# Optimization experiments

Measured on AMD Instinct MI355X. Metric: run time of the kernel, lower is better.

## Reference

```python
import jax, jax.numpy as jnp
import numpy as np

EPS = 1e-8

def setup_inputs() -> dict:
    key = jax.random.key(0)
    k1, k2 = jax.random.split(key)
    B, D, H, W, K = 32, 256, 64, 64, 64
    X = jax.random.normal(k1, (B, D, H, W), dtype=jnp.float32)
    std1 = 1.0 / float(np.sqrt(K * D))
    codewords = jax.random.uniform(k2, (K, D), dtype=jnp.float32, minval=-std1, maxval=std1)
    return {"X": X, "codewords": codewords}

def reference(X, codewords):
    B, D = X.shape[0], X.shape[1]
    # (B, D, H, W) -> (B, N, D)
    Xf = X.reshape(B, D, -1).transpose(0, 2, 1)
    # pairwise cosine similarity: normalize then matmul -> (B, N, K)
    Xn = Xf / jnp.maximum(jnp.linalg.norm(Xf, axis=-1, keepdims=True), EPS)
    Cn = codewords / jnp.maximum(jnp.linalg.norm(codewords, axis=-1, keepdims=True), EPS)
    L = jnp.einsum('bnd,kd->bnk', Xn, Cn)
    A = jax.nn.softmax(L, axis=2)
    # aggregate: E[b,k,d] = sum_n A[b,n,k] * (Xf[b,n,d] - C[k,d])
    # expressed without materializing the (B,N,K,D) residual tensor:
    E = jnp.einsum('bnk,bnd->bkd', A, Xf) - A.sum(axis=1)[:, :, None] * codewords[None, :, :]
    return E
```

## Files before the change

kernel.cpp:

```cpp
#include <hip/hip_runtime.h>
#include <hip/hip_bf16.h>
#include <math.h>

#define BB 32
#define DD 256
#define NN 4096
#define KK 64
#define EPSV 1e-8f
#define XSTR 264

typedef __attribute__((ext_vector_type(8))) short short8;
typedef __attribute__((ext_vector_type(4))) float f32x4;

__device__ __forceinline__ unsigned int bf16pair(float a, float b) {
    __hip_bfloat162 h = __float22bfloat162_rn(make_float2(a, b));
    return *(unsigned int*)&h;
}
__device__ __forceinline__ unsigned short bf16one(float a) {
    unsigned int ua = __float_as_uint(a);
    ua += 0x7fffu + ((ua >> 16) & 1u);
    return (unsigned short)(ua >> 16);
}

__device__ __forceinline__ void stage_group(int dbase, int n4, const float4* rr,
                                            unsigned short* xnd_s, unsigned short* xdn_s,
                                            f32x4& ssn) {
    float4 r0 = rr[0], r1 = rr[1], r2 = rr[2], r3 = rr[3];
    ssn.x = fmaf(r0.x, r0.x, ssn.x); ssn.x = fmaf(r1.x, r1.x, ssn.x);
    ssn.x = fmaf(r2.x, r2.x, ssn.x); ssn.x = fmaf(r3.x, r3.x, ssn.x);
    ssn.y = fmaf(r0.y, r0.y, ssn.y); ssn.y = fmaf(r1.y, r1.y, ssn.y);
    ssn.y = fmaf(r2.y, r2.y, ssn.y); ssn.y = fmaf(r3.y, r3.y, ssn.y);
    ssn.z = fmaf(r0.z, r0.z, ssn.z); ssn.z = fmaf(r1.z, r1.z, ssn.z);
    ssn.z = fmaf(r2.z, r2.z, ssn.z); ssn.z = fmaf(r3.z, r3.z, ssn.z);
    ssn.w = fmaf(r0.w, r0.w, ssn.w); ssn.w = fmaf(r1.w, r1.w, ssn.w);
    ssn.w = fmaf(r2.w, r2.w, ssn.w); ssn.w = fmaf(r3.w, r3.w, ssn.w);
#pragma unroll
    for (int j = 0; j < 4; j++) {
        int d = dbase + j;
        uint2 u;
        u.x = bf16pair(rr[j].x, rr[j].y);
        u.y = bf16pair(rr[j].z, rr[j].w);
        *(uint2*)(xdn_s + d * 64 + ((((n4 >> 3) ^ (d & 7)) << 3) | (n4 & 7))) = u;
    }
    {
        float col[4][4] = {{r0.x, r1.x, r2.x, r3.x},
                           {r0.y, r1.y, r2.y, r3.y},
                           {r0.z, r1.z, r2.z, r3.z},
                           {r0.w, r1.w, r2.w, r3.w}};
#pragma unroll
        for (int j = 0; j < 4; j++) {
            int n = n4 + j;
            uint2 u;
            u.x = bf16pair(col[j][0], col[j][1]);
            u.y = bf16pair(col[j][2], col[j][3]);
            int blk = (dbase >> 3) ^ ((n >> 2) & 3);
            *(uint2*)(xnd_s + n * XSTR + (blk << 3) + (dbase & 7)) = u;
        }
    }
}

__global__ __launch_bounds__(256, 2) void k_fused(const float* __restrict__ X,
                                                  const float* __restrict__ C,
                                                  float* __restrict__ P,
                                                  float* __restrict__ Sp) {
    __shared__ unsigned short xnd_s[64 * XSTR];
    __shared__ unsigned short xdn_s[DD * 64];
    __shared__ unsigned short at_s[KK * 72];
    __shared__ float rn4[4 * 64];
    __shared__ float red_s[4 * 64];

    int t = threadIdx.x;
    int b = blockIdx.x >> 4, chunk = blockIdx.x & 15;
    int w = t >> 6, lane = t & 63, c = lane & 15, g = lane >> 4;
    int q = t >> 4;
    int n4 = c * 4;

    const float* Xb = X + (size_t)b * DD * NN + chunk * 256;

    float4 pre[8];
#pragma unroll
    for (int i = 0; i < 2; i++) {
        const float* xb = Xb + (size_t)(q * 4 + 64 * i) * NN + n4;
#pragma unroll
        for (int j = 0; j < 4; j++) pre[i * 4 + j] = *(const float4*)(xb + (size_t)j * NN);
    }

    short8 cnf[8];
    {
        int k = 16 * w + c;
        const float* cp = C + k * DD;
        float4 v0[8], v1[8];
        float ss = 0.f;
#pragma unroll
        for (int ks = 0; ks < 8; ks++) {
            v0[ks] = *(const float4*)(cp + 32 * ks + 8 * g);
            v1[ks] = *(const float4*)(cp + 32 * ks + 8 * g + 4);
            ss = fmaf(v0[ks].x, v0[ks].x, ss); ss = fmaf(v0[ks].y, v0[ks].y, ss);
            ss = fmaf(v0[ks].z, v0[ks].z, ss); ss = fmaf(v0[ks].w, v0[ks].w, ss);
            ss = fmaf(v1[ks].x, v1[ks].x, ss); ss = fmaf(v1[ks].y, v1[ks].y, ss);
            ss = fmaf(v1[ks].z, v1[ks].z, ss); ss = fmaf(v1[ks].w, v1[ks].w, ss);
        }
        ss += __shfl_xor(ss, 16);
        ss += __shfl_xor(ss, 32);
        float r = 1.f / fmaxf(sqrtf(ss), EPSV);
#pragma unroll
        for (int ks = 0; ks < 8; ks++) {
            uint4 u;
            u.x = bf16pair(v0[ks].x * r, v0[ks].y * r);
            u.y = bf16pair(v0[ks].z * r, v0[ks].w * r);
            u.z = bf16pair(v1[ks].x * r, v1[ks].y * r);
            u.w = bf16pair(v1[ks].z * r, v1[ks].w * r);
            cnf[ks] = *(short8*)&u;
        }
    }

    f32x4 eacc[4][4];
#pragma unroll
    for (int dt = 0; dt < 4; dt++)
#pragma unroll
        for (int kt = 0; kt < 4; kt++) eacc[dt][kt] = (f32x4){0.f, 0.f, 0.f, 0.f};
    float s_acc[4] = {0.f, 0.f, 0.f, 0.f};

    for (int p = 0; p < 4; p++) {
        float4 cur[8];
#pragma unroll
        for (int i = 0; i < 2; i++) {
            const float* xb = Xb + (size_t)(q * 4 + 64 * (2 + i)) * NN + p * 64 + n4;
#pragma unroll
            for (int j = 0; j < 4; j++) cur[i * 4 + j] = *(const float4*)(xb + (size_t)j * NN);
        }
        __syncthreads();

        f32x4 ssn = (f32x4){0.f, 0.f, 0.f, 0.f};
#pragma unroll
        for (int i = 0; i < 2; i++)
            stage_group(q * 4 + 64 * i, n4, &pre[i * 4], xnd_s, xdn_s, ssn);

        if (p < 3) {
#pragma unroll
            for (int i = 0; i < 2; i++) {
                const float* xb = Xb + (size_t)(q * 4 + 64 * i) * NN + (p + 1) * 64 + n4;
#pragma unroll
                for (int j = 0; j < 4; j++) pre[i * 4 + j] = *(const float4*)(xb + (size_t)j * NN);
            }
        }

#pragma unroll
        for (int i = 0; i < 2; i++)
            stage_group(q * 4 + 64 * (2 + i), n4, &cur[i * 4], xnd_s, xdn_s, ssn);

        ssn.x += __shfl_xor(ssn.x, 16); ssn.x += __shfl_xor(ssn.x, 32);
        ssn.y += __shfl_xor(ssn.y, 16); ssn.y += __shfl_xor(ssn.y, 32);
        ssn.z += __shfl_xor(ssn.z, 16); ssn.z += __shfl_xor(ssn.z, 32);
        ssn.w += __shfl_xor(ssn.w, 16); ssn.w += __shfl_xor(ssn.w, 32);
        if (g == 0) *(f32x4*)(rn4 + w * 64 + n4) = ssn;

        __syncthreads();

        f32x4 lacc[4];
#pragma unroll
        for (int nt = 0; nt < 4; nt++) lacc[nt] = (f32x4){0.f, 0.f, 0.f, 0.f};
#pragma unroll
        for (int ks = 0; ks < 8; ks++) {
            short8 af = cnf[ks];
#pragma unroll
            for (int nt = 0; nt < 4; nt++) {
                int n = nt * 16 + c;
                short8 bf = *(const short8*)(xnd_s + n * XSTR +
                                             (((4 * ks + g) ^ ((n >> 2) & 3)) << 3));
                lacc[nt] = __builtin_amdgcn_mfma_f32_16x16x32_bf16(af, bf, lacc[nt], 0, 0, 0);
            }
        }

        float lv[4][4];
#pragma unroll
        for (int nt = 0; nt < 4; nt++) {
            int n = nt * 16 + c;
            float ssq = rn4[n] + rn4[64 + n] + rn4[128 + n] + rn4[192 + n];
            float rn = 1.f / fmaxf(sqrtf(ssq), EPSV);
            float s = 0.f;
#pragma unroll
            for (int r = 0; r < 4; r++) {
                lv[nt][r] = __expf(lacc[nt][r] * rn);
                s += lv[nt][r];
            }
            s += __shfl_xor(s, 16);
            s += __shfl_xor(s, 32);
            if (g == 0) red_s[w * 64 + n] = s;
        }
        __syncthreads();

#pragma unroll
        for (int nt = 0; nt < 4; nt++) {
            int n = nt * 16 + c;
            float denom = red_s[n] + red_s[64 + n] + red_s[128 + n] + red_s[192 + n];
            float inv = 1.f / denom;
#pragma unroll
            for (int r = 0; r < 4; r++) {
                float a = lv[nt][r] * inv;
                s_acc[r] += a;
                int k = 16 * w + 4 * g + r;
                at_s[k * 72 + ((((n >> 3) ^ (k & 7)) << 3) | (n & 7))] = bf16one(a);
            }
        }
        __syncthreads();

#pragma unroll
        for (int ks2 = 0; ks2 < 2; ks2++) {
            short8 bk[4];
#pragma unroll
            for (int kt = 0; kt < 4; kt++) {
                int k = kt * 16 + c;
                bk[kt] = *(const short8*)(at_s + k * 72 + (((4 * ks2 + g) ^ (k & 7)) << 3));
            }
#pragma unroll
            for (int dt = 0; dt < 4; dt++) {
                int d = w * 64 + dt * 16 + c;
                short8 af = *(const short8*)(xdn_s + d * 64 + (((4 * ks2 + g) ^ (d & 7)) << 3));
#pragma unroll
                for (int kt = 0; kt < 4; kt++)
                    eacc[dt][kt] =
                        __builtin_amdgcn_mfma_f32_16x16x32_bf16(af, bk[kt], eacc[dt][kt], 0, 0, 0);
            }
        }
    }

    float* Pb = P + (size_t)blockIdx.x * (DD * KK);
#pragma unroll
    for (int dt = 0; dt < 4; dt++)
#pragma unroll
        for (int kt = 0; kt < 4; kt++) {
            int k = kt * 16 + c;
            int d0 = w * 64 + dt * 16 + 4 * g;
            *(f32x4*)(Pb + (size_t)k * DD + d0) = eacc[dt][kt];
        }
#pragma unroll
    for (int r = 0; r < 4; r++) {
        float v = s_acc[r];
        v += __shfl_xor(v, 1);
        v += __shfl_xor(v, 2);
        v += __shfl_xor(v, 4);
        v += __shfl_xor(v, 8);
        if (c == 0) Sp[blockIdx.x * 64 + 16 * w + 4 * g + r] = v;
    }
}

__global__ __launch_bounds__(256) void k_fin(const float* __restrict__ P,
                                             const float* __restrict__ Sp,
                                             const float* __restrict__ C,
                                             float* __restrict__ out) {
    int idx = blockIdx.x * 256 + threadIdx.x;
    int b = idx >> 12;
    int r = idx & 4095;
    int k = r >> 6;
    int d0 = (r & 63) * 4;
    const float* Pp = P + (size_t)b * 16 * (DD * KK) + k * DD + d0;
    const float* Sb = Sp + b * 16 * 64 + k;
    f32x4 e0 = (f32x4){0.f, 0.f, 0.f, 0.f};
    f32x4 e1 = (f32x4){0.f, 0.f, 0.f, 0.f};
    float s0 = 0.f, s1 = 0.f;
#pragma unroll
    for (int cc = 0; cc < 16; cc += 2) {
        f32x4 p0 = *(const f32x4*)(Pp + (size_t)cc * (DD * KK));
        f32x4 p1 = *(const f32x4*)(Pp + (size_t)(cc + 1) * (DD * KK));
        e0 += p0;
        e1 += p1;
        s0 += Sb[cc * 64];
        s1 += Sb[(cc + 1) * 64];
    }
    f32x4 cv = *(const f32x4*)(C + k * DD + d0);
    f32x4 e = e0 + e1;
    float s = s0 + s1;
    f32x4 o;
    o.x = e.x - s * cv.x;
    o.y = e.y - s * cv.y;
    o.z = e.z - s * cv.z;
    o.w = e.w - s * cv.w;
    *(f32x4*)(out + (size_t)(b * 64 + k) * DD + d0) = o;
}

extern "C" void kernel_launch(void* const* d_in, const int* in_sizes, int n_in,
                              void* d_out, int out_size, void* d_ws, size_t ws_size,
                              hipStream_t stream) {
    const float* X = (const float*)d_in[0];
    const float* C = (const float*)d_in[1];
    float* out = (float*)d_out;
    unsigned char* ws = (unsigned char*)d_ws;

    float* Sp = (float*)ws;
    float* P = (float*)(ws + 131072);

    k_fused<<<512, 256, 0, stream>>>(X, C, P, Sp);
    k_fin<<<512, 256, 0, stream>>>(P, Sp, C, out);
}
```

Baseline: 212.0 us.

## Double threads per block to 512, splitting work across eight waves

```diff
diff --git a/kernel.cpp b/kernel.cpp
--- a/kernel.cpp
+++ b/kernel.cpp
@@ -59,35 +59,35 @@
     }
 }
 
-__global__ __launch_bounds__(256, 2) void k_fused(const float* __restrict__ X,
+__global__ __launch_bounds__(512, 4) void k_fused(const float* __restrict__ X,
                                                   const float* __restrict__ C,
                                                   float* __restrict__ P,
                                                   float* __restrict__ Sp) {
     __shared__ unsigned short xnd_s[64 * XSTR];
     __shared__ unsigned short xdn_s[DD * 64];
     __shared__ unsigned short at_s[KK * 72];
-    __shared__ float rn4[4 * 64];
-    __shared__ float red_s[4 * 64];
+    __shared__ float rn4[8 * 64];
+    __shared__ float red_s[8 * 64];
 
     int t = threadIdx.x;
     int b = blockIdx.x >> 4, chunk = blockIdx.x & 15;
     int w = t >> 6, lane = t & 63, c = lane & 15, g = lane >> 4;
-    int q = t >> 4;
+    int q2 = t >> 4;
     int n4 = c * 4;
+    int kw = w & 3, nh = w >> 2;
 
     const float* Xb = X + (size_t)b * DD * NN + chunk * 256;
 
-    float4 pre[8];
-#pragma unroll
-    for (int i = 0; i < 2; i++) {
-        const float* xb = Xb + (size_t)(q * 4 + 64 * i) * NN + n4;
-#pragma unroll
-        for (int j = 0; j < 4; j++) pre[i * 4 + j] = *(const float4*)(xb + (size_t)j * NN);
+    float4 pre[4];
+    {
+        const float* xb = Xb + (size_t)(q2 * 4) * NN + n4;
+#pragma unroll
+        for (int j = 0; j < 4; j++) pre[j] = *(const float4*)(xb + (size_t)j * NN);
     }
 
     short8 cnf[8];
     {
-        int k = 16 * w + c;
+        int k = 16 * kw + c;
         const float* cp = C + k * DD;
         float4 v0[8], v1[8];
         float ss = 0.f;
@@ -114,40 +114,32 @@
         }
     }
 
-    f32x4 eacc[4][4];
-#pragma unroll
-    for (int dt = 0; dt < 4; dt++)
+    f32x4 eacc[2][4];
+#pragma unroll
+    for (int dt = 0; dt < 2; dt++)
 #pragma unroll
         for (int kt = 0; kt < 4; kt++) eacc[dt][kt] = (f32x4){0.f, 0.f, 0.f, 0.f};
     float s_acc[4] = {0.f, 0.f, 0.f, 0.f};
 
     for (int p = 0; p < 4; p++) {
-        float4 cur[8];
-#pragma unroll
-        for (int i = 0; i < 2; i++) {
-            const float* xb = Xb + (size_t)(q * 4 + 64 * (2 + i)) * NN + p * 64 + n4;
-#pragma unroll
-            for (int j = 0; j < 4; j++) cur[i * 4 + j] = *(const float4*)(xb + (size_t)j * NN);
+        float4 cur[4];
+        {
+            const float* xb = Xb + (size_t)(q2 * 4 + 128) * NN + p * 64 + n4;
+#pragma unroll
+            for (int j = 0; j < 4; j++) cur[j] = *(const float4*)(xb + (size_t)j * NN);
         }
         __syncthreads();
 
         f32x4 ssn = (f32x4){0.f, 0.f, 0.f, 0.f};
-#pragma unroll
-        for (int i = 0; i < 2; i++)
-            stage_group(q * 4 + 64 * i, n4, &pre[i * 4], xnd_s, xdn_s, ssn);
+        stage_group(q2 * 4, n4, pre, xnd_s, xdn_s, ssn);
 
         if (p < 3) {
-#pragma unroll
-            for (int i = 0; i < 2; i++) {
-                const float* xb = Xb + (size_t)(q * 4 + 64 * i) * NN + (p + 1) * 64 + n4;
-#pragma unroll
-                for (int j = 0; j < 4; j++) pre[i * 4 + j] = *(const float4*)(xb + (size_t)j * NN);
-            }
-        }
-
-#pragma unroll
-        for (int i = 0; i < 2; i++)
-            stage_group(q * 4 + 64 * (2 + i), n4, &cur[i * 4], xnd_s, xdn_s, ssn);
+            const float* xb = Xb + (size_t)(q2 * 4) * NN + (p + 1) * 64 + n4;
+#pragma unroll
+            for (int j = 0; j < 4; j++) pre[j] = *(const float4*)(xb + (size_t)j * NN);
+        }
+
+        stage_group(q2 * 4 + 128, n4, cur, xnd_s, xdn_s, ssn);
 
         ssn.x += __shfl_xor(ssn.x, 16); ssn.x += __shfl_xor(ssn.x, 32);
         ssn.y += __shfl_xor(ssn.y, 16); ssn.y += __shfl_xor(ssn.y, 32);
@@ -157,26 +149,27 @@
 
         __syncthreads();
 
-        f32x4 lacc[4];
-#pragma unroll
-        for (int nt = 0; nt < 4; nt++) lacc[nt] = (f32x4){0.f, 0.f, 0.f, 0.f};
+        f32x4 lacc[2];
+#pragma unroll
+        for (int nt = 0; nt < 2; nt++) lacc[nt] = (f32x4){0.f, 0.f, 0.f, 0.f};
 #pragma unroll
         for (int ks = 0; ks < 8; ks++) {
             short8 af = cnf[ks];
 #pragma unroll
-            for (int nt = 0; nt < 4; nt++) {
-                int n = nt * 16 + c;
+            for (int nt = 0; nt < 2; nt++) {
+                int n = 32 * nh + nt * 16 + c;
                 short8 bf = *(const short8*)(xnd_s + n * XSTR +
                                              (((4 * ks + g) ^ ((n >> 2) & 3)) << 3));
                 lacc[nt] = __builtin_amdgcn_mfma_f32_16x16x32_bf16(af, bf, lacc[nt], 0, 0, 0);
             }
         }
 
-        float lv[4][4];
-#pragma unroll
-        for (int nt = 0; nt < 4; nt++) {
-            int n = nt * 16 + c;
-            float ssq = rn4[n] + rn4[64 + n] + rn4[128 + n] + rn4[192 + n];
+        float lv[2][4];
+#pragma unroll
+        for (int nt = 0; nt < 2; nt++) {
+            int n = 32 * nh + nt * 16 + c;
+            float ssq = rn4[n] + rn4[64 + n] + rn4[128 + n] + rn4[192 + n] +
+                        rn4[256 + n] + rn4[320 + n] + rn4[384 + n] + rn4[448 + n];
             float rn = 1.f / fmaxf(sqrtf(ssq), EPSV);
             float s = 0.f;
 #pragma unroll
@@ -191,15 +184,16 @@
         __syncthreads();
 
 #pragma unroll
-        for (int nt = 0; nt < 4; nt++) {
-            int n = nt * 16 + c;
-            float denom = red_s[n] + red_s[64 + n] + red_s[128 + n] + red_s[192 + n];
+        for (int nt = 0; nt < 2; nt++) {
+            int n = 32 * nh + nt * 16 + c;
+            float denom = red_s[(4 * nh + 0) * 64 + n] + red_s[(4 * nh + 1) * 64 + n] +
+                          red_s[(4 * nh + 2) * 64 + n] + red_s[(4 * nh + 3) * 64 + n];
             float inv = 1.f / denom;
 #pragma unroll
             for (int r = 0; r < 4; r++) {
                 float a = lv[nt][r] * inv;
                 s_acc[r] += a;
-                int k = 16 * w + 4 * g + r;
+                int k = 16 * kw + 4 * g + r;
                 at_s[k * 72 + ((((n >> 3) ^ (k & 7)) << 3) | (n & 7))] = bf16one(a);
             }
         }
@@ -214,8 +208,8 @@
                 bk[kt] = *(const short8*)(at_s + k * 72 + (((4 * ks2 + g) ^ (k & 7)) << 3));
             }
 #pragma unroll
-            for (int dt = 0; dt < 4; dt++) {
-                int d = w * 64 + dt * 16 + c;
+            for (int dt = 0; dt < 2; dt++) {
+                int d = 32 * w + dt * 16 + c;
                 short8 af = *(const short8*)(xdn_s + d * 64 + (((4 * ks2 + g) ^ (d & 7)) << 3));
 #pragma unroll
                 for (int kt = 0; kt < 4; kt++)
@@ -227,13 +221,14 @@
 
     float* Pb = P + (size_t)blockIdx.x * (DD * KK);
 #pragma unroll
-    for (int dt = 0; dt < 4; dt++)
+    for (int dt = 0; dt < 2; dt++)
 #pragma unroll
         for (int kt = 0; kt < 4; kt++) {
             int k = kt * 16 + c;
-            int d0 = w * 64 + dt * 16 + 4 * g;
+            int d0 = 32 * w + dt * 16 + 4 * g;
             *(f32x4*)(Pb + (size_t)k * DD + d0) = eacc[dt][kt];
         }
+
 #pragma unroll
     for (int r = 0; r < 4; r++) {
         float v = s_acc[r];
@@ -241,7 +236,13 @@
         v += __shfl_xor(v, 2);
         v += __shfl_xor(v, 4);
         v += __shfl_xor(v, 8);
-        if (c == 0) Sp[blockIdx.x * 64 + 16 * w + 4 * g + r] = v;
+        if (c == 0) red_s[w * 64 + 16 * kw + 4 * g + r] = v;
+    }
+    __syncthreads();
+    if (t < KK) {
+        int k = t;
+        int kw2 = k >> 4;
+        Sp[blockIdx.x * 64 + k] = red_s[kw2 * 64 + k] + red_s[(kw2 + 4) * 64 + k];
     }
 }
 
@@ -290,6 +291,6 @@
     float* Sp = (float*)ws;
     float* P = (float*)(ws + 131072);
 
-    k_fused<<<512, 256, 0, stream>>>(X, C, P, Sp);
+    k_fused<<<512, 512, 0, stream>>>(X, C, P, Sp);
     k_fin<<<512, 256, 0, stream>>>(P, Sp, C, out);
 }
```

Measured after the change: 229.8 us. 1.08x slower.
